# Kernel optimization log

Hardware: AMD Instinct MI355X
Metric: run time of the kernel (lower is better)

Reference implementation:

```python
import jax, jax.numpy as jnp
import numpy as np
import math

B, S, H, NH = 2, 2048, 2048, 16
HD = H // NH
LAYER_NUMBER = 5
NORM_FACTOR = math.sqrt(HD) * LAYER_NUMBER  # sqrt(head_dim) * coeff
BETA = 1.0 / LAYER_NUMBER
SCALE = float(LAYER_NUMBER)  # ScaledSoftmax scale = coeff
MASK_VALUE = -10000.0


def setup_inputs() -> dict:
    key = jax.random.key(0)
    ks = jax.random.split(key, 6)
    inv_sqrt_h = 1.0 / math.sqrt(H)
    return {
        "hidden_states": jax.random.normal(ks[0], (B, S, H), jnp.float32),
        "alibi": jax.random.normal(ks[1], (NH, 1, S), jnp.float32) * 0.1,
        "w_qkv": jax.random.normal(ks[2], (3 * H, H), jnp.float32) * inv_sqrt_h,
        "b_qkv": jax.random.normal(ks[3], (3 * H,), jnp.float32) * 0.02,
        "w_dense": jax.random.normal(ks[4], (H, H), jnp.float32) * inv_sqrt_h,
        "b_dense": jax.random.normal(ks[5], (H,), jnp.float32) * 0.02,
        "attention_mask": jnp.ones((B, S), jnp.int32),
    }


def reference(hidden_states, alibi, w_qkv, b_qkv, w_dense, b_dense, attention_mask):
    b, s, h = hidden_states.shape
    # QKV projection: [b, s, 3h] -> [b, s, nh, 3*hd] -> split
    mixed = hidden_states @ w_qkv.T + b_qkv
    mixed = mixed.reshape(b, s, NH, 3 * HD)
    q, k, v = jnp.split(mixed, 3, axis=-1)  # each [b, s, nh, hd]

    # Faithful Megatron-style memory reinterpretation (row-major reshape),
    # exactly matching torch's .contiguous().view(s, b*nh, hd).
    q2 = jnp.swapaxes(q.reshape(s, b * NH, HD), 0, 1)  # [b*nh, q_len, hd]
    k2 = jnp.swapaxes(k.reshape(s, b * NH, HD), 0, 1)  # [b*nh, k_len, hd]
    v2 = jnp.swapaxes(v.reshape(s, b * NH, HD), 0, 1)  # [b*nh, k_len, hd]

    # baddbmm: alibi*beta + (q @ k^T)/norm_factor
    alibi_b = jnp.tile(alibi, (b, 1, 1))[: b * NH, :, :s]  # [b*nh, 1, k_len]
    scores = alibi_b * BETA + jnp.einsum("bqd,bkd->bqk", q2, k2) * (1.0 / NORM_FACTOR)
    scores = scores.reshape(b, NH, s, s)

    # ScaledSoftmax: scale then fused causal+padding mask fill, then softmax
    scores = scores * SCALE
    pad_bool = (1 - attention_mask).astype(bool)  # True where padded
    causal = jnp.tril(jnp.ones((s, s), dtype=bool))
    bad = pad_bool[:, None, :, None] | (~causal)[None, None, :, :]  # [b,1,s,s]
    scores = jnp.where(bad, MASK_VALUE, scores)
    probs = jax.nn.softmax(scores, axis=-1)  # [b, nh, s, s]

    # context = probs @ V with the same faithful reshapes
    probs_r = probs.reshape(b * NH, s, s)
    context = jnp.einsum("bqk,bkd->bqd", probs_r, v2)  # [b*nh, q_len, hd]
    context = context.reshape(b, NH, s, HD)
    context = jnp.transpose(context, (2, 0, 1, 3)).reshape(s, b, h)  # [s, b, h]

    out = context @ w_dense.T + b_dense  # [s, b, h]
    return jnp.swapaxes(out, 0, 1)  # [b, s, h]
```

## Files before the change

kernel.cpp:

```cpp
#include <hip/hip_runtime.h>

typedef unsigned short u16;
typedef __bf16  bf16x8 __attribute__((ext_vector_type(8)));
typedef float   f32x4  __attribute__((ext_vector_type(4)));
typedef u16     u16x8  __attribute__((ext_vector_type(8)));
typedef u16     u16x4  __attribute__((ext_vector_type(4)));

#define QSCALE 0.12751744545f

__device__ __forceinline__ u16 f2b(float f) {
    unsigned u = __float_as_uint(f);
    unsigned r = u + 0x7FFFu + ((u >> 16) & 1u);
    return (u16)(r >> 16);
}
__device__ __forceinline__ float b2f(u16 b) {
    return __uint_as_float(((unsigned)b) << 16);
}
__device__ __forceinline__ void async16(const u16* g, u16* l) {
    __builtin_amdgcn_global_load_lds(
        (__attribute__((address_space(1))) void*)(u16*)g,
        (__attribute__((address_space(3))) void*)l, 16, 0, 0);
}

__global__ void cvt_f32_bf16(const float* __restrict__ in, u16* __restrict__ out, int n4) {
    int i = blockIdx.x * blockDim.x + threadIdx.x;
    if (i >= n4) return;
    float4 f = ((const float4*)in)[i];
    u16x4 o;
    o[0] = f2b(f.x); o[1] = f2b(f.y); o[2] = f2b(f.z); o[3] = f2b(f.w);
    *(u16x4*)(out + (size_t)i * 4) = o;
}

__global__ void cvt_wqkv(const float* __restrict__ in, u16* __restrict__ out, int n4) {
    int i = blockIdx.x * blockDim.x + threadIdx.x;
    if (i >= n4) return;
    int row = i >> 9;
    float s = ((row % 384) < 128) ? QSCALE : 1.0f;
    float4 f = ((const float4*)in)[i];
    u16x4 o;
    o[0] = f2b(f.x * s); o[1] = f2b(f.y * s); o[2] = f2b(f.z * s); o[3] = f2b(f.w * s);
    *(u16x4*)(out + (size_t)i * 4) = o;
}

__global__ __launch_bounds__(512, 2) void gemm_qkv(
    const u16* __restrict__ A, const u16* __restrict__ B,
    const float* __restrict__ bias,
    u16* __restrict__ qb, u16* __restrict__ kb, u16* __restrict__ vb)
{
    constexpr int K  = 2048;
    constexpr int NS = K / 32;
    __shared__ u16 lds[65536];

    const int tid = threadIdx.x, wave = tid >> 6, lane = tid & 63;
    const int lm = lane & 15, lg = lane >> 4;
    const int wr = wave >> 2, wc = wave & 3;

    const int rbase = blockIdx.y * 256;
    const int cbase = blockIdx.x * 256;

    const int srl = lane >> 2;
    const int scs = ((lane & 3) ^ ((lane >> 3) & 3)) << 3;
    const u16* sl0;
    int lbase;
    {
        int qq = (wave & 3) * 4;
        if (wave < 4) { sl0 = A + (size_t)rbase * K; lbase = qq * 512; }
        else          { sl0 = B + (size_t)cbase * K; lbase = 8192 + qq * 512; }
        sl0 += (size_t)(qq * 16 + srl) * K + scs;
    }
    auto stage2 = [&](int s_, int c0) {
        int slot = (s_ & 3) * 16384;
        size_t k0 = (size_t)s_ * 32;
        for (int c = c0; c < c0 + 2; c++)
            async16(sl0 + (size_t)c * 16 * K + k0, &lds[slot + lbase + c * 512]);
    };

    const int coff = (lg ^ ((lm >> 1) & 3)) << 3;
    const int aoff = (wr * 128 + lm) * 32 + coff;
    const int boff = 8192 + (wc * 64 + lm) * 32 + coff;

    f32x4 acc[8][4];
    for (int m = 0; m < 8; m++)
        for (int n = 0; n < 4; n++)
            acc[m][n] = (f32x4){0.f, 0.f, 0.f, 0.f};

    stage2(0, 0); stage2(0, 2);
    stage2(1, 0); stage2(1, 2);
    stage2(2, 0); stage2(2, 2);
    asm volatile("s_waitcnt vmcnt(8)" ::: "memory");
    __builtin_amdgcn_s_barrier();

    for (int s = 0; s < NS; s++) {
        const u16* sl = &lds[(s & 3) * 16384];
        bf16x8 af[4], bf[4];

        for (int n = 0; n < 4; n++) bf[n] = *(const bf16x8*)&sl[boff + n * 512];
        for (int m = 0; m < 4; m++) af[m] = *(const bf16x8*)&sl[aoff + m * 512];
        if (s + 3 < NS) stage2(s + 3, 0);
        __builtin_amdgcn_s_barrier();
        __builtin_amdgcn_s_setprio(1);
        for (int m = 0; m < 4; m++)
            for (int n = 0; n < 4; n++)
                acc[m][n] = __builtin_amdgcn_mfma_f32_16x16x32_bf16(af[m], bf[n], acc[m][n], 0, 0, 0);
        __builtin_amdgcn_s_setprio(0);
        __builtin_amdgcn_s_barrier();

        for (int m = 0; m < 4; m++) af[m] = *(const bf16x8*)&sl[aoff + (m + 4) * 512];
        if (s + 3 < NS) stage2(s + 3, 2);
        __builtin_amdgcn_s_barrier();
        __builtin_amdgcn_s_setprio(1);
        for (int m = 0; m < 4; m++)
            for (int n = 0; n < 4; n++)
                acc[m + 4][n] = __builtin_amdgcn_mfma_f32_16x16x32_bf16(af[m], bf[n], acc[m + 4][n], 0, 0, 0);
        __builtin_amdgcn_s_setprio(0);

        if (s + 1 < NS) {
            if (s < NS - 3)       asm volatile("s_waitcnt vmcnt(8)" ::: "memory");
            else if (s == NS - 3) asm volatile("s_waitcnt vmcnt(4)" ::: "memory");
            else                  asm volatile("s_waitcnt vmcnt(0)" ::: "memory");
            __builtin_amdgcn_s_barrier();
        }
    }

    __syncthreads();

    const int ct   = (cbase >> 7) + (wc >> 1);
    const int nh   = ct / 3, part = ct - nh * 3;
    const int hd0  = (wc & 1) * 64;
    const int posb = (rbase >> 11) << 10;
    const int sblk = (rbase & 2047) + wr * 128;

    if (part < 2) {
        u16* dst0 = part ? kb : qb;
        const float bsc = part ? 1.0f : QSCALE;
        for (int n = 0; n < 4; n++) {
            int hd = hd0 + n * 16 + lm;
            float bv = bias[ct * 128 + hd] * bsc;
            for (int m = 0; m < 8; m++) {
                for (int r = 0; r < 4; r++) {
                    int s_  = sblk + m * 16 + lg * 4 + r;
                    int bn  = (s_ & 1) * 16 + nh;
                    int pos = posb + (s_ >> 1);
                    dst0[((size_t)(bn * 2048 + pos)) * 128 + hd] = f2b(acc[m][n][r] + bv);
                }
            }
        }
    } else {
        u16* scr = &lds[wave * 8192];
        for (int n = 0; n < 4; n++) {
            int hdl = n * 16 + lm;
            float bv = bias[ct * 128 + hd0 + hdl];
            for (int m = 0; m < 8; m++)
                for (int r = 0; r < 4; r++)
                    scr[(m * 16 + lg * 4 + r) * 64 + hdl] = f2b(acc[m][n][r] + bv);
        }
        int pos0 = posb + (sblk >> 1);
        for (int par = 0; par < 2; par++) {
            int bn = par * 16 + nh;
            u16* dst = vb + ((size_t)(bn * 128 + hd0 + lane)) * 2048 + pos0;
            for (int p8 = 0; p8 < 8; p8++) {
                u16x8 w;
                for (int e = 0; e < 8; e++)
                    w[e] = scr[(2 * (p8 * 8 + e) + par) * 64 + lane];
                *(u16x8*)(dst + p8 * 8) = w;
            }
        }
    }
}

__global__ __launch_bounds__(256) void gemm_bt(
    const u16* __restrict__ A, const u16* __restrict__ B,
    const float* __restrict__ bias, void* __restrict__ C,
    u16* __restrict__ qb, u16* __restrict__ kb, u16* __restrict__ vb,
    int M, int N, int K, int mode)
{
    __shared__ u16 smem[16384];
    u16* As = smem;
    u16* Bs = smem + 8192;

    int tid = threadIdx.x, wave = tid >> 6, lane = tid & 63;
    int lg = lane >> 4, lm = lane & 15;
    int wm = (wave & 1) * 64, wn = (wave >> 1) * 64;

    const u16* Ab = A + (size_t)(blockIdx.y * 128) * K;
    const u16* Bb = B + (size_t)(blockIdx.x * 128) * K;

    f32x4 acc[4][4];
    for (int i = 0; i < 4; i++)
        for (int j = 0; j < 4; j++)
            acc[i][j] = (f32x4){0.f, 0.f, 0.f, 0.f};

    int srow = (lane >> 2), skq = (lane & 3) * 8;

    for (int k0 = 0; k0 < K; k0 += 64) {
        __syncthreads();
        for (int cc = wave; cc < 16; cc += 4) {
            int p = cc >> 3, c = cc & 7;
            int row = c * 16 + srow;
            size_t off = (size_t)row * K + k0 + p * 32 + skq;
            async16(Ab + off, &As[p * 4096 + c * 512]);
            async16(Bb + off, &Bs[p * 4096 + c * 512]);
        }
        __syncthreads();

        for (int p = 0; p < 2; p++) {
            bf16x8 af[4], bf[4];
            for (int i = 0; i < 4; i++) af[i] = *(const bf16x8*)&As[p * 4096 + (wm + i * 16 + lm) * 32 + lg * 8];
            for (int j = 0; j < 4; j++) bf[j] = *(const bf16x8*)&Bs[p * 4096 + (wn + j * 16 + lm) * 32 + lg * 8];
            for (int i = 0; i < 4; i++)
                for (int j = 0; j < 4; j++)
                    acc[i][j] = __builtin_amdgcn_mfma_f32_16x16x32_bf16(af[i], bf[j], acc[i][j], 0, 0, 0);
        }
    }

    if (mode == 1) {
        for (int j = 0; j < 4; j++) {
            int col = blockIdx.x * 128 + wn + j * 16 + lm;
            float bv = bias[col];
            for (int i = 0; i < 4; i++) {
                int row0 = blockIdx.y * 128 + wm + i * 16 + lg * 4;
                for (int r = 0; r < 4; r++) {
                    int row = row0 + r;
                    int orow = ((row & 1) << 11) + (row >> 1);
                    ((float*)C)[(size_t)orow * N + col] = acc[i][j][r] + bv;
                }
            }
        }
        return;
    }
}

__global__ __launch_bounds__(256) void attn(
    const u16* __restrict__ qb, const u16* __restrict__ kb,
    const u16* __restrict__ vb, const float* __restrict__ alibi,
    u16* __restrict__ ctx)
{
    __shared__ u16 Ks[64 * 128];
    __shared__ u16 Vt[128 * 64];
    __shared__ u16 Ps[4][32 * 64];

    int bn = blockIdx.y;
    int tid = threadIdx.x, wave = tid >> 6, lane = tid & 63;
    int lg = lane >> 4, lm = lane & 15;
    const int rxor = (lm & 7) * 8;

    const float* al = alibi + (bn & 15) * 2048;

    int krow = tid >> 2, kq = (tid & 3) * 32;
    int vhd  = tid >> 1, vh2 = (tid & 1) * 32;
    const u16* ksrc0 = kb + (size_t)(bn * 2048 + krow) * 128 + kq;
    const u16* vsrc0 = vb + (size_t)(bn * 128 + vhd) * 2048 + vh2;
    const int kxor = (krow & 7) * 8;
    const int vxor = (vhd & 7) * 8;

    u16* ps = &Ps[wave][0];
    bf16x8 ones;
    {
        u16x8 t;
        for (int j = 0; j < 8; j++) t[j] = 0x3F80;
        ones = *(bf16x8*)&t;
    }

    for (int pass = 0; pass < 2; pass++) {
        int qtb = pass ? (15 - blockIdx.x) : blockIdx.x;
        int q0 = qtb * 128;
        int ktmax = 2 * qtb + 1;
        int qrow0 = q0 + wave * 32;

        bf16x8 qf[2][4];
        for (int f = 0; f < 2; f++) {
            const u16* qp = qb + ((size_t)bn * 2048 + qrow0 + f * 16 + lm) * 128 + lg * 8;
            for (int kc = 0; kc < 4; kc++) qf[f][kc] = *(const bf16x8*)(qp + kc * 32);
        }

        f32x4 o[2][9];
        for (int f = 0; f < 2; f++)
            for (int i = 0; i < 9; i++) o[f][i] = (f32x4){0.f, 0.f, 0.f, 0.f};

        u16x8 kreg[4], vreg[4];
        for (int i = 0; i < 4; i++) kreg[i] = *(const u16x8*)(ksrc0 + i * 8);
        for (int i = 0; i < 4; i++) vreg[i] = *(const u16x8*)(vsrc0 + i * 8);

        for (int kt = 0; kt <= ktmax; kt++) {
            int k0 = kt * 64;
            __syncthreads();
            {
                u16* d1 = &Ks[krow * 128];
                for (int i = 0; i < 4; i++) *(u16x8*)&d1[(kq + i * 8) ^ kxor] = kreg[i];
                u16* d2 = &Vt[vhd * 64];
                for (int i = 0; i < 4; i++) *(u16x8*)&d2[(vh2 + i * 8) ^ vxor] = vreg[i];
            }
            __syncthreads();

            if (kt < ktmax) {
                const u16* s1 = ksrc0 + (size_t)(kt + 1) * 64 * 128;
                const u16* s2 = vsrc0 + (kt + 1) * 64;
                for (int i = 0; i < 4; i++) kreg[i] = *(const u16x8*)(s1 + i * 8);
                for (int i = 0; i < 4; i++) vreg[i] = *(const u16x8*)(s2 + i * 8);
            }

            bool act = (k0 <= qrow0 + 31);
            if (act) {
                f32x4 sc[2][4];
                for (int tc = 0; tc < 4; tc++) {
                    const u16* kr = &Ks[(tc * 16 + lm) * 128];
                    bf16x8 krf[4];
                    for (int kc = 0; kc < 4; kc++)
                        krf[kc] = *(const bf16x8*)&kr[(kc * 32 + lg * 8) ^ rxor];
                    for (int f = 0; f < 2; f++) {
                        f32x4 a = (f32x4){0.f, 0.f, 0.f, 0.f};
                        for (int kc = 0; kc < 4; kc++)
                            a = __builtin_amdgcn_mfma_f32_16x16x32_bf16(qf[f][kc], krf[kc], a, 0, 0, 0);
                        sc[f][tc] = a;
                    }
                }

                bool dz = (kt >= 2 * qtb);
                for (int tc = 0; tc < 4; tc++) {
                    int kg = k0 + tc * 16 + lm;
                    float av = (al[kg] - 8.0f) * 1.4426950408889634f;
                    for (int f = 0; f < 2; f++) {
                        for (int r = 0; r < 4; r++) {
                            float v = sc[f][tc][r] + av;
                            if (dz && kg > qrow0 + f * 16 + lg * 4 + r) v = -3e38f;
                            int row = f * 16 + lg * 4 + r;
                            ps[row * 64 + ((tc * 16 + lm) ^ ((row & 7) * 8))] =
                                f2b(__builtin_amdgcn_exp2f(v));
                        }
                    }
                }

                for (int kc = 0; kc < 2; kc++) {
                    bf16x8 pf[2];
                    for (int f = 0; f < 2; f++)
                        pf[f] = *(const bf16x8*)&ps[(f * 16 + lm) * 64 + ((kc * 32 + lg * 8) ^ rxor)];
                    for (int i = 0; i < 8; i++) {
                        bf16x8 vf = *(const bf16x8*)&Vt[(i * 16 + lm) * 64 + ((kc * 32 + lg * 8) ^ rxor)];
                        for (int f = 0; f < 2; f++)
                            o[f][i] = __builtin_amdgcn_mfma_f32_16x16x32_bf16(pf[f], vf, o[f][i], 0, 0, 0);
                    }
                    for (int f = 0; f < 2; f++)
                        o[f][8] = __builtin_amdgcn_mfma_f32_16x16x32_bf16(pf[f], ones, o[f][8], 0, 0, 0);
                }
            }
        }

        for (int f = 0; f < 2; f++) {
            for (int r = 0; r < 4; r++) {
                float inv = 1.0f / o[f][8][r];
                int qg = qrow0 + f * 16 + lg * 4 + r;
                int row = qg * 2 + (bn >> 4);
                u16* crow = ctx + (size_t)row * 2048 + (bn & 15) * 128 + lm;
                for (int i = 0; i < 8; i++)
                    crow[i * 16] = f2b(o[f][i][r] * inv);
            }
        }
    }
}

extern "C" void kernel_launch(void* const* d_in, const int* in_sizes, int n_in,
                              void* d_out, int out_size, void* d_ws, size_t ws_size,
                              hipStream_t stream)
{
    const float* hs    = (const float*)d_in[0];
    const float* alibi = (const float*)d_in[1];
    const float* wqkv  = (const float*)d_in[2];
    const float* bqkv  = (const float*)d_in[3];
    const float* wd    = (const float*)d_in[4];
    const float* bd    = (const float*)d_in[5];
    float* out = (float*)d_out;

    char* ws = (char*)d_ws;
    u16* wqkv_b = (u16*)(ws + 0);
    u16* hs_b   = (u16*)(ws + 25165824);
    u16* ctx    = (u16*)(ws + 41943040);
    u16* wd_b   = wqkv_b;
    u16* qb     = (u16*)(ws + 92274688);
    u16* kb     = (u16*)(ws + 109051904);
    u16* vb     = (u16*)(ws + 125829120);

    cvt_f32_bf16<<<8192,  256, 0, stream>>>(hs,   hs_b,   2097152);
    cvt_wqkv   <<<12288, 256, 0, stream>>>(wqkv, wqkv_b, 3145728);

    gemm_qkv<<<dim3(24, 16), 512, 0, stream>>>(hs_b, wqkv_b, bqkv, qb, kb, vb);

    cvt_f32_bf16<<<4096, 256, 0, stream>>>(wd, wd_b, 1048576);

    attn<<<dim3(8, 32), 256, 0, stream>>>(qb, kb, vb, alibi, ctx);

    gemm_bt<<<dim3(16, 32), 256, 0, stream>>>(ctx, wd_b, bd, out,
                                              nullptr, nullptr, nullptr, 4096, 2048, 2048, 1);
}
```

Before: 411.6 us.

## Double-buffer attention K/V tiles via async global-to-LDS loads, split passes into blocks

The attention kernel now loads K and V tiles straight into LDS with global_load_lds into two ping-pong buffers. The next tile is prefetched while the current one is computed, which replaces the old register staging with its two block barriers per tile. The two causal passes that each block used to run in sequence are now spread over twice as many blocks (16x32 grid), with the light and heavy query tiles on separate blocks, to raise parallelism. In exchange LDS use doubles, which may cut occupancy, and the swizzled async layout depends on hand-written vmcnt waits being correct.

```diff
diff --git a/kernel.cpp b/kernel.cpp
--- a/kernel.cpp
+++ b/kernel.cpp
@@ -12,9 +12,6 @@
     unsigned u = __float_as_uint(f);
     unsigned r = u + 0x7FFFu + ((u >> 16) & 1u);
     return (u16)(r >> 16);
-}
-__device__ __forceinline__ float b2f(u16 b) {
-    return __uint_as_float(((unsigned)b) << 16);
 }
 __device__ __forceinline__ void async16(const u16* g, u16* l) {
     __builtin_amdgcn_global_load_lds(
@@ -171,8 +168,7 @@
 __global__ __launch_bounds__(256) void gemm_bt(
     const u16* __restrict__ A, const u16* __restrict__ B,
     const float* __restrict__ bias, void* __restrict__ C,
-    u16* __restrict__ qb, u16* __restrict__ kb, u16* __restrict__ vb,
-    int M, int N, int K, int mode)
+    int M, int N, int K)
 {
     __shared__ u16 smem[16384];
     u16* As = smem;
@@ -213,20 +209,17 @@
         }
     }
 
-    if (mode == 1) {
-        for (int j = 0; j < 4; j++) {
-            int col = blockIdx.x * 128 + wn + j * 16 + lm;
-            float bv = bias[col];
-            for (int i = 0; i < 4; i++) {
-                int row0 = blockIdx.y * 128 + wm + i * 16 + lg * 4;
-                for (int r = 0; r < 4; r++) {
-                    int row = row0 + r;
-                    int orow = ((row & 1) << 11) + (row >> 1);
-                    ((float*)C)[(size_t)orow * N + col] = acc[i][j][r] + bv;
-                }
-            }
-        }
-        return;
+    for (int j = 0; j < 4; j++) {
+        int col = blockIdx.x * 128 + wn + j * 16 + lm;
+        float bv = bias[col];
+        for (int i = 0; i < 4; i++) {
+            int row0 = blockIdx.y * 128 + wm + i * 16 + lg * 4;
+            for (int r = 0; r < 4; r++) {
+                int row = row0 + r;
+                int orow = ((row & 1) << 11) + (row >> 1);
+                ((float*)C)[(size_t)orow * N + col] = acc[i][j][r] + bv;
+            }
+        }
     }
 }
 
@@ -235,23 +228,42 @@
     const u16* __restrict__ vb, const float* __restrict__ alibi,
     u16* __restrict__ ctx)
 {
-    __shared__ u16 Ks[64 * 128];
-    __shared__ u16 Vt[128 * 64];
+    __shared__ u16 Ks2[2][64 * 128];
+    __shared__ u16 Vt2[2][128 * 64];
     __shared__ u16 Ps[4][32 * 64];
 
-    int bn = blockIdx.y;
-    int tid = threadIdx.x, wave = tid >> 6, lane = tid & 63;
-    int lg = lane >> 4, lm = lane & 15;
+    const int x = blockIdx.x, y = blockIdx.y;
+    const int bn = (y & 15) | ((x & 1) << 4);
+    const int qh = (x >> 1) & 7;
+    const int qt = (y >> 4) ? (15 - qh) : qh;
+    const int q0 = qt * 128;
+    const int ktmax = 2 * qt + 1;
+
+    const int tid = threadIdx.x, wave = tid >> 6, lane = tid & 63;
+    const int lg = lane >> 4, lm = lane & 15;
     const int rxor = (lm & 7) * 8;
+    const int qrow0 = q0 + wave * 32;
 
     const float* al = alibi + (bn & 15) * 2048;
 
-    int krow = tid >> 2, kq = (tid & 3) * 32;
-    int vhd  = tid >> 1, vh2 = (tid & 1) * 32;
-    const u16* ksrc0 = kb + (size_t)(bn * 2048 + krow) * 128 + kq;
-    const u16* vsrc0 = vb + (size_t)(bn * 128 + vhd) * 2048 + vh2;
-    const int kxor = (krow & 7) * 8;
-    const int vxor = (vhd & 7) * 8;
+    const int krl = lane >> 4;
+    const u16* Kbase = kb + ((size_t)bn * 2048 + 16 * wave + krl) * 128;
+    const int kco0 = ((lane & 15) ^ krl) * 8;
+    const int kco1 = ((lane & 15) ^ (4 + krl)) * 8;
+    const int vl = lane >> 3;
+    const u16* Vbase = vb + ((size_t)(bn * 128 + 32 * wave) + vl) * 2048
+                          + (((lane & 7) ^ vl) * 8);
+
+    auto stage = [&](int buf, int kt) {
+        size_t k0 = (size_t)kt * 64;
+        u16* kd = &Ks2[buf][16 * wave * 128];
+        for (int i = 0; i < 4; i++)
+            async16(Kbase + (k0 + 4 * i) * 128 + ((i & 1) ? kco1 : kco0),
+                    kd + 4 * i * 128);
+        u16* vd = &Vt2[buf][32 * wave * 64];
+        for (int i = 0; i < 4; i++)
+            async16(Vbase + (size_t)i * 16384 + k0, vd + 8 * i * 64);
+    };
 
     u16* ps = &Ps[wave][0];
     bf16x8 ones;
@@ -261,99 +273,87 @@
         ones = *(bf16x8*)&t;
     }
 
-    for (int pass = 0; pass < 2; pass++) {
-        int qtb = pass ? (15 - blockIdx.x) : blockIdx.x;
-        int q0 = qtb * 128;
-        int ktmax = 2 * qtb + 1;
-        int qrow0 = q0 + wave * 32;
-
-        bf16x8 qf[2][4];
-        for (int f = 0; f < 2; f++) {
-            const u16* qp = qb + ((size_t)bn * 2048 + qrow0 + f * 16 + lm) * 128 + lg * 8;
-            for (int kc = 0; kc < 4; kc++) qf[f][kc] = *(const bf16x8*)(qp + kc * 32);
-        }
-
-        f32x4 o[2][9];
-        for (int f = 0; f < 2; f++)
-            for (int i = 0; i < 9; i++) o[f][i] = (f32x4){0.f, 0.f, 0.f, 0.f};
-
-        u16x8 kreg[4], vreg[4];
-        for (int i = 0; i < 4; i++) kreg[i] = *(const u16x8*)(ksrc0 + i * 8);
-        for (int i = 0; i < 4; i++) vreg[i] = *(const u16x8*)(vsrc0 + i * 8);
-
-        for (int kt = 0; kt <= ktmax; kt++) {
-            int k0 = kt * 64;
-            __syncthreads();
-            {
-                u16* d1 = &Ks[krow * 128];
-                for (int i = 0; i < 4; i++) *(u16x8*)&d1[(kq + i * 8) ^ kxor] = kreg[i];
-                u16* d2 = &Vt[vhd * 64];
-                for (int i = 0; i < 4; i++) *(u16x8*)&d2[(vh2 + i * 8) ^ vxor] = vreg[i];
-            }
-            __syncthreads();
-
-            if (kt < ktmax) {
-                const u16* s1 = ksrc0 + (size_t)(kt + 1) * 64 * 128;
-                const u16* s2 = vsrc0 + (kt + 1) * 64;
-                for (int i = 0; i < 4; i++) kreg[i] = *(const u16x8*)(s1 + i * 8);
-                for (int i = 0; i < 4; i++) vreg[i] = *(const u16x8*)(s2 + i * 8);
-            }
-
-            bool act = (k0 <= qrow0 + 31);
-            if (act) {
-                f32x4 sc[2][4];
-                for (int tc = 0; tc < 4; tc++) {
-                    const u16* kr = &Ks[(tc * 16 + lm) * 128];
-                    bf16x8 krf[4];
+    bf16x8 qf[2][4];
+    for (int f = 0; f < 2; f++) {
+        const u16* qp = qb + ((size_t)bn * 2048 + qrow0 + f * 16 + lm) * 128 + lg * 8;
+        for (int kc = 0; kc < 4; kc++) qf[f][kc] = *(const bf16x8*)(qp + kc * 32);
+    }
+
+    f32x4 o[2][9];
+    for (int f = 0; f < 2; f++)
+        for (int i = 0; i < 9; i++) o[f][i] = (f32x4){0.f, 0.f, 0.f, 0.f};
+
+    stage(0, 0);
+
+    for (int kt = 0; kt <= ktmax; kt++) {
+        int buf = kt & 1;
+        if (kt < ktmax) {
+            stage(buf ^ 1, kt + 1);
+            asm volatile("s_waitcnt vmcnt(8)" ::: "memory");
+        } else {
+            asm volatile("s_waitcnt vmcnt(0)" ::: "memory");
+        }
+        __builtin_amdgcn_s_barrier();
+
+        int k0 = kt * 64;
+        bool act = (k0 <= qrow0 + 31);
+        if (act) {
+            const u16* KsB = &Ks2[buf][0];
+            const u16* VtB = &Vt2[buf][0];
+
+            f32x4 sc[2][4];
+            for (int tc = 0; tc < 4; tc++) {
+                const u16* kr = &KsB[(tc * 16 + lm) * 128];
+                bf16x8 krf[4];
+                for (int kc = 0; kc < 4; kc++)
+                    krf[kc] = *(const bf16x8*)&kr[(kc * 32 + lg * 8) ^ rxor];
+                for (int f = 0; f < 2; f++) {
+                    f32x4 a = (f32x4){0.f, 0.f, 0.f, 0.f};
                     for (int kc = 0; kc < 4; kc++)
-                        krf[kc] = *(const bf16x8*)&kr[(kc * 32 + lg * 8) ^ rxor];
-                    for (int f = 0; f < 2; f++) {
-                        f32x4 a = (f32x4){0.f, 0.f, 0.f, 0.f};
-                        for (int kc = 0; kc < 4; kc++)
-                            a = __builtin_amdgcn_mfma_f32_16x16x32_bf16(qf[f][kc], krf[kc], a, 0, 0, 0);
-                        sc[f][tc] = a;
+                        a = __builtin_amdgcn_mfma_f32_16x16x32_bf16(qf[f][kc], krf[kc], a, 0, 0, 0);
+                    sc[f][tc] = a;
+                }
+            }
+
+            bool dz = (kt >= 2 * qt);
+            for (int tc = 0; tc < 4; tc++) {
+                int kg = k0 + tc * 16 + lm;
+                float av = (al[kg] - 8.0f) * 1.4426950408889634f;
+                for (int f = 0; f < 2; f++) {
+                    for (int r = 0; r < 4; r++) {
+                        float v = sc[f][tc][r] + av;
+                        if (dz && kg > qrow0 + f * 16 + lg * 4 + r) v = -3e38f;
+                        int row = f * 16 + lg * 4 + r;
+                        ps[row * 64 + ((tc * 16 + lm) ^ ((row & 7) * 8))] =
+                            f2b(__builtin_amdgcn_exp2f(v));
                     }
                 }
-
-                bool dz = (kt >= 2 * qtb);
-                for (int tc = 0; tc < 4; tc++) {
-                    int kg = k0 + tc * 16 + lm;
-                    float av = (al[kg] - 8.0f) * 1.4426950408889634f;
-                    for (int f = 0; f < 2; f++) {
-                        for (int r = 0; r < 4; r++) {
-                            float v = sc[f][tc][r] + av;
-                            if (dz && kg > qrow0 + f * 16 + lg * 4 + r) v = -3e38f;
-                            int row = f * 16 + lg * 4 + r;
-                            ps[row * 64 + ((tc * 16 + lm) ^ ((row & 7) * 8))] =
-                                f2b(__builtin_amdgcn_exp2f(v));
-                        }
-                    }
+            }
+
+            for (int kc = 0; kc < 2; kc++) {
+                bf16x8 pf[2];
+                for (int f = 0; f < 2; f++)
+                    pf[f] = *(const bf16x8*)&ps[(f * 16 + lm) * 64 + ((kc * 32 + lg * 8) ^ rxor)];
+                for (int i = 0; i < 8; i++) {
+                    bf16x8 vf = *(const bf16x8*)&VtB[(i * 16 + lm) * 64 + ((kc * 32 + lg * 8) ^ rxor)];
+                    for (int f = 0; f < 2; f++)
+                        o[f][i] = __builtin_amdgcn_mfma_f32_16x16x32_bf16(pf[f], vf, o[f][i], 0, 0, 0);
                 }
-
-                for (int kc = 0; kc < 2; kc++) {
-                    bf16x8 pf[2];
-                    for (int f = 0; f < 2; f++)
-                        pf[f] = *(const bf16x8*)&ps[(f * 16 + lm) * 64 + ((kc * 32 + lg * 8) ^ rxor)];
-                    for (int i = 0; i < 8; i++) {
-                        bf16x8 vf = *(const bf16x8*)&Vt[(i * 16 + lm) * 64 + ((kc * 32 + lg * 8) ^ rxor)];
-                        for (int f = 0; f < 2; f++)
-                            o[f][i] = __builtin_amdgcn_mfma_f32_16x16x32_bf16(pf[f], vf, o[f][i], 0, 0, 0);
-                    }
-                    for (int f = 0; f < 2; f++)
-                        o[f][8] = __builtin_amdgcn_mfma_f32_16x16x32_bf16(pf[f], ones, o[f][8], 0, 0, 0);
-                }
-            }
-        }
-
-        for (int f = 0; f < 2; f++) {
-            for (int r = 0; r < 4; r++) {
-                float inv = 1.0f / o[f][8][r];
-                int qg = qrow0 + f * 16 + lg * 4 + r;
-                int row = qg * 2 + (bn >> 4);
-                u16* crow = ctx + (size_t)row * 2048 + (bn & 15) * 128 + lm;
-                for (int i = 0; i < 8; i++)
-                    crow[i * 16] = f2b(o[f][i][r] * inv);
-            }
+                for (int f = 0; f < 2; f++)
+                    o[f][8] = __builtin_amdgcn_mfma_f32_16x16x32_bf16(pf[f], ones, o[f][8], 0, 0, 0);
+            }
+        }
+        __builtin_amdgcn_s_barrier();
+    }
+
+    for (int f = 0; f < 2; f++) {
+        for (int r = 0; r < 4; r++) {
+            float inv = 1.0f / o[f][8][r];
+            int qg = qrow0 + f * 16 + lg * 4 + r;
+            int row = qg * 2 + (bn >> 4);
+            u16* crow = ctx + (size_t)row * 2048 + (bn & 15) * 128 + lm;
+            for (int i = 0; i < 8; i++)
+                crow[i * 16] = f2b(o[f][i][r] * inv);
         }
     }
 }
@@ -386,8 +386,7 @@
 
     cvt_f32_bf16<<<4096, 256, 0, stream>>>(wd, wd_b, 1048576);
 
-    attn<<<dim3(8, 32), 256, 0, stream>>>(qb, kb, vb, alibi, ctx);
-
-    gemm_bt<<<dim3(16, 32), 256, 0, stream>>>(ctx, wd_b, bd, out,
-                                              nullptr, nullptr, nullptr, 4096, 2048, 2048, 1);
-}
+    attn<<<dim3(16, 32), 256, 0, stream>>>(qb, kb, vb, alibi, ctx);
+
+    gemm_bt<<<dim3(16, 32), 256, 0, stream>>>(ctx, wd_b, bd, out, 4096, 2048, 2048);
+}
```

Measured after the change: 401.8 us. 2.4% less time.
